# Optimization experiments

Measured on AMD Instinct MI355X. Metric: run time of the kernel, lower is better.

The kernel has to match this reference:

```python
import jax, jax.numpy as jnp
import numpy as np

E = 8       # num_experts
K = 2       # top_k
N = 16384   # tokens
H = 2048    # hidden_dim
B = 128     # bottleneck_dim
EPS = 1e-6


def setup_inputs() -> dict:
    key = jax.random.key(0)
    ks = jax.random.split(key, 8)
    x = jax.random.normal(ks[0], (N, H), dtype=jnp.float32)
    skin_probs = jax.random.uniform(ks[1], (N, 3), dtype=jnp.float32)
    # routers (torch Linear weight layout: [out, in])
    W_img = jax.random.normal(ks[2], (E, H), dtype=jnp.float32) * 0.02
    W_skin = jax.random.normal(ks[3], (E, 3), dtype=jnp.float32) * 0.02
    # stacked expert params: Linear(H->B) then Linear(B->H)
    W1 = jax.random.normal(ks[4], (E, B, H), dtype=jnp.float32) * 0.02
    b1 = jax.random.normal(ks[5], (E, B), dtype=jnp.float32) * 0.02
    W2 = jax.random.normal(ks[6], (E, H, B), dtype=jnp.float32) * 0.02
    b2 = jax.random.normal(ks[7], (E, H), dtype=jnp.float32) * 0.02
    return {"x": x, "skin_probs": skin_probs, "W_img": W_img, "W_skin": W_skin,
            "W1": W1, "b1": b1, "W2": W2, "b2": b2}


def reference(x, skin_probs, W_img, W_skin, W1, b1, W2, b2):
    # router
    router_logits = x @ W_img.T + skin_probs @ W_skin.T          # [N, E]
    router_probs = jax.nn.softmax(router_logits, axis=-1)        # [N, E]
    top_v, top_i = jax.lax.top_k(router_probs, K)                 # [N, K]
    top_v = top_v / (top_v.sum(axis=-1, keepdims=True) + EPS)
    sel = jax.nn.one_hot(top_i, E, dtype=x.dtype)                 # [N, K, E], 0/1
    w = (sel * top_v[..., None]).sum(axis=1)                      # [N, E] combine weights (0 if not selected)
    # experts, dense-equivalent combine: out = sum_e w[n,e] * (relu(x W1_e^T + b1_e) W2_e^T + b2_e)
    h = jax.nn.relu(jnp.einsum('nh,ebh->neb', x, W1) + b1)        # [N, E, B]
    moe = jnp.einsum('neb,ehb->nh', h * w[:, :, None], W2) + w @ b2  # [N, H]
    out = x + moe
    # aux load-balancing loss
    mean_prob = router_probs.mean(axis=0)                         # [E]
    mean_freq = sel.sum(axis=1).mean(axis=0)                      # [E]
    aux_loss = (mean_prob * mean_freq).sum() * E
    return out, aux_loss
```

## Files before the change

### kernel.cpp

```cpp
#include <hip/hip_runtime.h>

#define N_TOK 16384
#define HD    2048
#define BD    128
#define NE    8
#define KEXT  1088

typedef float  f32x4  __attribute__((ext_vector_type(4)));
typedef __bf16 bf16x8 __attribute__((ext_vector_type(8)));
typedef unsigned short u16;
typedef unsigned short u16x4 __attribute__((ext_vector_type(4)));

__device__ __forceinline__ u16 f2bf(float f) {
  union { float f; unsigned u; } v; v.f = f;
  unsigned u = v.u;
  return (u16)((u + 0x7FFFu + ((u >> 16) & 1u)) >> 16);
}

__device__ __forceinline__ void gload16(const void* g, void* l) {
  __builtin_amdgcn_global_load_lds(
      (const __attribute__((address_space(1))) void*)g,
      (__attribute__((address_space(3))) void*)l, 16, 0, 0);
}

__global__ void init_aux_k(float* p) {
  if (threadIdx.x < 16) p[threadIdx.x] = 0.f;
}

__global__ __launch_bounds__(256) void conv_w1_k(const float* __restrict__ W1,
                                                 u16* __restrict__ W1b) {
  int i = (blockIdx.x * 256 + threadIdx.x) * 4;
  float4 v = *(const float4*)(W1 + i);
  u16x4 o; o.x = f2bf(v.x); o.y = f2bf(v.y); o.z = f2bf(v.z); o.w = f2bf(v.w);
  *(u16x4*)(W1b + i) = o;
}

__global__ __launch_bounds__(256) void conv_w2_k(const float* __restrict__ W2,
                                                 const float* __restrict__ b2,
                                                 u16* __restrict__ Bt2) {
  int i4 = (blockIdx.x * 256 + threadIdx.x) * 4;
  int h = i4 / KEXT, j0 = i4 % KEXT;
  u16x4 o;
  #pragma unroll
  for (int c = 0; c < 4; c++) {
    int j = j0 + c;
    float v;
    if (j < 1024) {
      int e = j >> 7, b = j & 127;
      v = W2[((size_t)e * HD + h) * BD + b];
    } else if (j < 1032) {
      v = b2[(size_t)(j - 1024) * HD + h];
    } else {
      v = 0.f;
    }
    if (c == 0) o.x = f2bf(v); else if (c == 1) o.y = f2bf(v);
    else if (c == 2) o.z = f2bf(v); else o.w = f2bf(v);
  }
  *(u16x4*)(Bt2 + i4) = o;
}

__global__ __launch_bounds__(256)
void router_k(const float* __restrict__ x, const float* __restrict__ skin,
              const float* __restrict__ Wimg, const float* __restrict__ Wskin,
              u16* __restrict__ xbf, float* __restrict__ wout,
              u16* __restrict__ h2, float* __restrict__ psum,
              float* __restrict__ cnt) {
  __shared__ float lw[NE * HD];
  int t = threadIdx.x;
  for (int i = t; i < NE * HD; i += 256) lw[i] = Wimg[i];
  __syncthreads();
  int l = t & 63, wv = t >> 6;
  float pacc = 0.f, cacc = 0.f;

  for (int it = 0; it < 4; it++) {
    int n = blockIdx.x * 16 + wv * 4 + it;
    float acc[NE];
    #pragma unroll
    for (int e = 0; e < NE; e++) acc[e] = 0.f;
    const float4* xr = (const float4*)(x + (size_t)n * HD);
    #pragma unroll
    for (int j = 0; j < 8; j++) {
      float4 xv = xr[j * 64 + l];
      u16x4 o; o.x = f2bf(xv.x); o.y = f2bf(xv.y); o.z = f2bf(xv.z); o.w = f2bf(xv.w);
      *(u16x4*)(xbf + (size_t)n * HD + j * 256 + l * 4) = o;
      #pragma unroll
      for (int e = 0; e < NE; e++) {
        const float* wr_ = &lw[e * HD + j * 256 + l * 4];
        acc[e] += xv.x * wr_[0] + xv.y * wr_[1] + xv.z * wr_[2] + xv.w * wr_[3];
      }
    }
    float logit[NE];
    #pragma unroll
    for (int e = 0; e < NE; e++) {
      float v = acc[e];
      for (int off = 32; off >= 1; off >>= 1) v += __shfl_xor(v, off);
      logit[e] = v + skin[n * 3 + 0] * Wskin[e * 3 + 0]
                   + skin[n * 3 + 1] * Wskin[e * 3 + 1]
                   + skin[n * 3 + 2] * Wskin[e * 3 + 2];
    }
    float mx = logit[0];
    #pragma unroll
    for (int e = 1; e < NE; e++) mx = fmaxf(mx, logit[e]);
    float p[NE], s = 0.f;
    #pragma unroll
    for (int e = 0; e < NE; e++) { p[e] = expf(logit[e] - mx); s += p[e]; }
    float inv = 1.f / s;
    #pragma unroll
    for (int e = 0; e < NE; e++) p[e] *= inv;
    int i1 = 0; float v1 = p[0];
    #pragma unroll
    for (int e = 1; e < NE; e++) if (p[e] > v1) { v1 = p[e]; i1 = e; }
    int i2 = -1; float v2 = -1.f;
    #pragma unroll
    for (int e = 0; e < NE; e++) if (e != i1 && p[e] > v2) { v2 = p[e]; i2 = e; }
    float denom = v1 + v2 + 1e-6f;
    float w1v = v1 / denom, w2v = v2 / denom;
    float wl = (l == i1) ? w1v : ((l == i2) ? w2v : 0.f);
    if (l < NE) wout[(size_t)n * NE + l] = wl;
    h2[(size_t)n * KEXT + 1024 + l] = (l < NE) ? f2bf(wl) : (u16)0;
    if (l < NE) pacc += p[l];
    if (l == i1 || l == i2) cacc += 1.f;
  }
  __syncthreads();
  float* red = lw;
  if (t < 16) red[t] = 0.f;
  __syncthreads();
  if (l < NE) { atomicAdd(&red[l], pacc); atomicAdd(&red[NE + l], cacc); }
  __syncthreads();
  if (t < 8)       atomicAdd(&psum[t], red[t]);
  else if (t < 16) atomicAdd(&cnt[t - 8], red[t]);
}

template <int EPI>
__global__ __launch_bounds__(256)
void gemm_bt(const u16* __restrict__ A, int lda,
             const u16* __restrict__ Bt, int ldb,
             int K, int NB, int chunk,
             const float* __restrict__ b1, const float* __restrict__ w,
             u16* __restrict__ Hout,
             const float* __restrict__ xres, float* __restrict__ out) {
  __shared__ u16 lA[128 * 64];
  __shared__ u16 lB[128 * 64];
  int xcd = blockIdx.x & 7, idxw = blockIdx.x >> 3;
  int lin = xcd * chunk + idxw;
  int bn = lin % NB, bm = lin / NB;

  int t = threadIdx.x;
  int l = t & 63, wv = t >> 6;
  int wr = wv >> 1, wc = wv & 1;
  int r = t >> 3, c8 = (t & 7) * 8;

  const u16* Ag = A + (size_t)(bm * 128 + r) * lda + c8;
  const u16* Bg = Bt + (size_t)(bn * 128 + r) * ldb + c8;
  u16* lAp = &lA[r * 64 + c8];
  u16* lBp = &lB[r * 64 + c8];

  f32x4 acc[4][4];
  #pragma unroll
  for (int m = 0; m < 4; m++)
    #pragma unroll
    for (int n = 0; n < 4; n++) acc[m][n] = (f32x4){0.f, 0.f, 0.f, 0.f};

  for (int k0 = 0; k0 < K; k0 += 64) {
    #pragma unroll
    for (int i = 0; i < 4; i++) {
      gload16(Ag + (size_t)i * 32 * lda + k0, lAp + i * 32 * 64);
      gload16(Bg + (size_t)i * 32 * ldb + k0, lBp + i * 32 * 64);
    }
    __syncthreads();
    #pragma unroll
    for (int kk = 0; kk < 64; kk += 32) {
      bf16x8 a[4], b[4];
      #pragma unroll
      for (int m = 0; m < 4; m++)
        a[m] = *(const bf16x8*)&lA[(wr * 64 + m * 16 + (l & 15)) * 64 + kk + (l >> 4) * 8];
      #pragma unroll
      for (int n = 0; n < 4; n++)
        b[n] = *(const bf16x8*)&lB[(wc * 64 + n * 16 + (l & 15)) * 64 + kk + (l >> 4) * 8];
      #pragma unroll
      for (int m = 0; m < 4; m++)
        #pragma unroll
        for (int n = 0; n < 4; n++)
          acc[m][n] = __builtin_amdgcn_mfma_f32_16x16x32_bf16(a[m], b[n], acc[m][n], 0, 0, 0);
    }
    __syncthreads();
  }

  int row0 = bm * 128 + wr * 64 + (l >> 4) * 4;
  int col0 = bn * 128 + wc * 64 + (l & 15);
  if (EPI == 1) {
    #pragma unroll
    for (int n = 0; n < 4; n++) {
      int col = col0 + n * 16;
      float b1v = b1[col];
      #pragma unroll
      for (int m = 0; m < 4; m++) {
        #pragma unroll
        for (int j = 0; j < 4; j++) {
          int row = row0 + m * 16 + j;
          float v = acc[m][n][j] + b1v;
          v = v > 0.f ? v : 0.f;
          v *= w[(size_t)row * NE + bn];
          Hout[(size_t)row * KEXT + col] = f2bf(v);
        }
      }
    }
  } else {
    #pragma unroll
    for (int m = 0; m < 4; m++) {
      #pragma unroll
      for (int j = 0; j < 4; j++) {
        int row = row0 + m * 16 + j;
        const float* xr = xres + (size_t)row * HD;
        float* orow = out + (size_t)row * HD;
        #pragma unroll
        for (int n = 0; n < 4; n++) {
          int col = col0 + n * 16;
          orow[col] = acc[m][n][j] + xr[col];
        }
      }
    }
  }
}

__global__ void aux_fin_k(const float* __restrict__ psum,
                          const float* __restrict__ cnt,
                          float* __restrict__ out) {
  if (threadIdx.x == 0) {
    float a = 0.f;
    for (int e = 0; e < NE; e++)
      a += (psum[e] / (float)N_TOK) * (cnt[e] / (float)N_TOK);
    out[(size_t)N_TOK * HD] = a * (float)NE;
  }
}

extern "C" void kernel_launch(void* const* d_in, const int* in_sizes, int n_in,
                              void* d_out, int out_size, void* d_ws, size_t ws_size,
                              hipStream_t stream) {
  const float* x     = (const float*)d_in[0];
  const float* skin  = (const float*)d_in[1];
  const float* Wimg  = (const float*)d_in[2];
  const float* Wskin = (const float*)d_in[3];
  const float* W1    = (const float*)d_in[4];
  const float* b1    = (const float*)d_in[5];
  const float* W2    = (const float*)d_in[6];
  const float* b2    = (const float*)d_in[7];
  float* out = (float*)d_out;

  char* ws = (char*)d_ws;
  u16*   xbf  = (u16*)(ws);
  float* wout = (float*)(ws + 67108864);
  u16*   h2   = (u16*)(ws + 67633152);
  u16*   W1b  = (u16*)(ws + 103284736);
  u16*   Bt2  = (u16*)(ws + 107479040);
  float* aux  = (float*)(ws + 111935488);
  float* psum = aux;
  float* cnt  = aux + 8;

  init_aux_k<<<1, 64, 0, stream>>>(aux);
  conv_w1_k<<<(NE * BD * HD) / (256 * 4), 256, 0, stream>>>(W1, W1b);
  conv_w2_k<<<(HD * KEXT) / (256 * 4), 256, 0, stream>>>(W2, b2, Bt2);
  router_k<<<N_TOK / 16, 256, 0, stream>>>(x, skin, Wimg, Wskin, xbf, wout, h2,
                                           psum, cnt);
  aux_fin_k<<<1, 64, 0, stream>>>(psum, cnt, out);
  gemm_bt<1><<<(N_TOK / 128) * (1024 / 128), 256, 0, stream>>>(
      xbf, HD, W1b, HD, HD, 1024 / 128, ((N_TOK / 128) * (1024 / 128)) / 8,
      b1, wout, h2, nullptr, nullptr);
  gemm_bt<2><<<(N_TOK / 128) * (HD / 128), 256, 0, stream>>>(
      h2, KEXT, Bt2, KEXT, KEXT, HD / 128, ((N_TOK / 128) * (HD / 128)) / 8,
      nullptr, nullptr, nullptr, x, out);
}
```

Before: 578.2 us.

## Swizzle GEMM LDS tiles and halve router LDS footprint for occupancy

The GEMM now XOR-swizzles the 16-byte chunk column by row when staging A/B tiles into LDS. The fragment reads apply the matching swizzle, which is meant to remove bank conflicts on the bf16x8 MFMA operand loads. The router kernel stages the 64KB router weight in two 32KB halves and keeps per-token accumulators across both halves, with launch bounds raised to allow more resident blocks. The trade-off is extra barriers and more registers in the router.

```diff
diff --git a/kernel.cpp b/kernel.cpp
--- a/kernel.cpp
+++ b/kernel.cpp
@@ -59,40 +59,55 @@
   *(u16x4*)(Bt2 + i4) = o;
 }
 
-__global__ __launch_bounds__(256)
+__global__ __launch_bounds__(256, 4)
 void router_k(const float* __restrict__ x, const float* __restrict__ skin,
               const float* __restrict__ Wimg, const float* __restrict__ Wskin,
               u16* __restrict__ xbf, float* __restrict__ wout,
               u16* __restrict__ h2, float* __restrict__ psum,
               float* __restrict__ cnt) {
-  __shared__ float lw[NE * HD];
+  __shared__ float lw[NE * 1024];
+  __shared__ float red[16];
   int t = threadIdx.x;
-  for (int i = t; i < NE * HD; i += 256) lw[i] = Wimg[i];
-  __syncthreads();
   int l = t & 63, wv = t >> 6;
+  float acc[4][NE];
+  #pragma unroll
+  for (int it = 0; it < 4; it++)
+    #pragma unroll
+    for (int e = 0; e < NE; e++) acc[it][e] = 0.f;
+
+  for (int half = 0; half < 2; half++) {
+    __syncthreads();
+    for (int i = t; i < NE * 256; i += 256) {
+      int e = i >> 8, c4 = (i & 255) * 4;
+      *(float4*)&lw[e * 1024 + c4] = *(const float4*)&Wimg[(size_t)e * HD + half * 1024 + c4];
+    }
+    __syncthreads();
+    for (int it = 0; it < 4; it++) {
+      int n = blockIdx.x * 16 + wv * 4 + it;
+      const float* xr = x + (size_t)n * HD + half * 1024;
+      u16* xo = xbf + (size_t)n * HD + half * 1024;
+      #pragma unroll
+      for (int j = 0; j < 4; j++) {
+        int base = j * 256 + l * 4;
+        float4 xv = *(const float4*)&xr[base];
+        u16x4 o; o.x = f2bf(xv.x); o.y = f2bf(xv.y); o.z = f2bf(xv.z); o.w = f2bf(xv.w);
+        *(u16x4*)&xo[base] = o;
+        #pragma unroll
+        for (int e = 0; e < NE; e++) {
+          const float* wr_ = &lw[e * 1024 + base];
+          acc[it][e] += xv.x * wr_[0] + xv.y * wr_[1] + xv.z * wr_[2] + xv.w * wr_[3];
+        }
+      }
+    }
+  }
+
   float pacc = 0.f, cacc = 0.f;
-
   for (int it = 0; it < 4; it++) {
     int n = blockIdx.x * 16 + wv * 4 + it;
-    float acc[NE];
-    #pragma unroll
-    for (int e = 0; e < NE; e++) acc[e] = 0.f;
-    const float4* xr = (const float4*)(x + (size_t)n * HD);
-    #pragma unroll
-    for (int j = 0; j < 8; j++) {
-      float4 xv = xr[j * 64 + l];
-      u16x4 o; o.x = f2bf(xv.x); o.y = f2bf(xv.y); o.z = f2bf(xv.z); o.w = f2bf(xv.w);
-      *(u16x4*)(xbf + (size_t)n * HD + j * 256 + l * 4) = o;
-      #pragma unroll
-      for (int e = 0; e < NE; e++) {
-        const float* wr_ = &lw[e * HD + j * 256 + l * 4];
-        acc[e] += xv.x * wr_[0] + xv.y * wr_[1] + xv.z * wr_[2] + xv.w * wr_[3];
-      }
-    }
     float logit[NE];
     #pragma unroll
     for (int e = 0; e < NE; e++) {
-      float v = acc[e];
+      float v = acc[it][e];
       for (int off = 32; off >= 1; off >>= 1) v += __shfl_xor(v, off);
       logit[e] = v + skin[n * 3 + 0] * Wskin[e * 3 + 0]
                    + skin[n * 3 + 1] * Wskin[e * 3 + 1]
@@ -122,7 +137,6 @@
     if (l == i1 || l == i2) cacc += 1.f;
   }
   __syncthreads();
-  float* red = lw;
   if (t < 16) red[t] = 0.f;
   __syncthreads();
   if (l < NE) { atomicAdd(&red[l], pacc); atomicAdd(&red[NE + l], cacc); }
@@ -148,12 +162,16 @@
   int t = threadIdx.x;
   int l = t & 63, wv = t >> 6;
   int wr = wv >> 1, wc = wv & 1;
-  int r = t >> 3, c8 = (t & 7) * 8;
-
-  const u16* Ag = A + (size_t)(bm * 128 + r) * lda + c8;
-  const u16* Bg = Bt + (size_t)(bn * 128 + r) * ldb + c8;
-  u16* lAp = &lA[r * 64 + c8];
-  u16* lBp = &lB[r * 64 + c8];
+  int r = t >> 3;
+  int cl = (t & 7) * 8;
+  int cs = (((t & 7) ^ (r & 7))) * 8;
+
+  const u16* Ag = A + (size_t)(bm * 128 + r) * lda + cs;
+  const u16* Bg = Bt + (size_t)(bn * 128 + r) * ldb + cs;
+  u16* lAp = &lA[r * 64 + cl];
+  u16* lBp = &lB[r * 64 + cl];
+
+  int swz = (l & 7) << 4;
 
   f32x4 acc[4][4];
   #pragma unroll
@@ -170,13 +188,19 @@
     __syncthreads();
     #pragma unroll
     for (int kk = 0; kk < 64; kk += 32) {
+      int cb = (kk + (l >> 4) * 8) * 2;
+      int co = cb ^ swz;
       bf16x8 a[4], b[4];
       #pragma unroll
-      for (int m = 0; m < 4; m++)
-        a[m] = *(const bf16x8*)&lA[(wr * 64 + m * 16 + (l & 15)) * 64 + kk + (l >> 4) * 8];
-      #pragma unroll
-      for (int n = 0; n < 4; n++)
-        b[n] = *(const bf16x8*)&lB[(wc * 64 + n * 16 + (l & 15)) * 64 + kk + (l >> 4) * 8];
+      for (int m = 0; m < 4; m++) {
+        int Ra = wr * 64 + m * 16 + (l & 15);
+        a[m] = *(const bf16x8*)((const char*)lA + Ra * 128 + co);
+      }
+      #pragma unroll
+      for (int n = 0; n < 4; n++) {
+        int Rb = wc * 64 + n * 16 + (l & 15);
+        b[n] = *(const bf16x8*)((const char*)lB + Rb * 128 + co);
+      }
       #pragma unroll
       for (int m = 0; m < 4; m++)
         #pragma unroll
```

New measurement: 717.3 us. +24.1%, slower.
